# Kernel tuning notes

Measured on AMD Instinct MI355X. Metric: run time of the kernel, lower is better.

Reference implementation:

```python
import jax, jax.numpy as jnp
import numpy as np
import math

VOCAB, D, H, L = 32000, 1024, 16, 4
HD = D // H
DFF = 4 * D
EPS = 1e-5


def setup_inputs() -> dict:
    key = jax.random.key(0)
    ks = jax.random.split(key, 20)
    B, T = 4, 1024
    s = 0.02
    inp = {
        'inputs': jax.random.randint(ks[0], (B, T), 0, VOCAB),
        'emb_table': jax.random.normal(ks[1], (VOCAB, D), jnp.float32) * s,
        'Wq': jax.random.normal(ks[2], (L, D, D), jnp.float32) * s,
        'bq': jnp.zeros((L, D), jnp.float32),
        'Wk': jax.random.normal(ks[3], (L, D, D), jnp.float32) * s,
        'bk': jnp.zeros((L, D), jnp.float32),
        'Wv': jax.random.normal(ks[4], (L, D, D), jnp.float32) * s,
        'bv': jnp.zeros((L, D), jnp.float32),
        'Wo': jax.random.normal(ks[5], (L, D, D), jnp.float32) * s,
        'bo': jnp.zeros((L, D), jnp.float32),
        'ln1_g': jnp.ones((L, D), jnp.float32),
        'ln1_b': jnp.zeros((L, D), jnp.float32),
        'W1': jax.random.normal(ks[6], (L, D, DFF), jnp.float32) * s,
        'b1': jnp.zeros((L, DFF), jnp.float32),
        'W2': jax.random.normal(ks[7], (L, DFF, D), jnp.float32) * s,
        'b2': jnp.zeros((L, D), jnp.float32),
        'ln2_g': jnp.ones((L, D), jnp.float32),
        'ln2_b': jnp.zeros((L, D), jnp.float32),
    }
    return inp


def _layernorm(x, g, b):
    mu = jnp.mean(x, axis=-1, keepdims=True)
    var = jnp.mean(jnp.square(x - mu), axis=-1, keepdims=True)
    return (x - mu) * jax.lax.rsqrt(var + EPS) * g + b


def _pos_emb(T):
    pos = jnp.arange(T, dtype=jnp.float32)[:, None]          # [T,1]
    div = jnp.exp(jnp.arange(0, D, 2, dtype=jnp.float32) * (-math.log(10000.0) / D))
    pe = jnp.zeros((T, D), jnp.float32)
    pe = pe.at[:, 0::2].set(jnp.sin(pos * div))
    pe = pe.at[:, 1::2].set(jnp.cos(pos * div))
    return pe


def reference(inputs, emb_table, Wq, bq, Wk, bk, Wv, bv, Wo, bo,
              ln1_g, ln1_b, W1, b1, W2, b2, ln2_g, ln2_b):
    B, T = inputs.shape
    x = emb_table[inputs] + _pos_emb(T)[None, :, :]          # [B,T,D]
    causal = jnp.tril(jnp.ones((T, T), bool))                # [T,T]
    scale = 1.0 / math.sqrt(HD)
    for l in range(L):
        q = (x @ Wq[l] + bq[l]).reshape(B, T, H, HD)
        k = (x @ Wk[l] + bk[l]).reshape(B, T, H, HD)
        v = (x @ Wv[l] + bv[l]).reshape(B, T, H, HD)
        scores = jnp.einsum('bqhd,bkhd->bhqk', q, k) * scale
        scores = jnp.where(causal, scores, -jnp.inf)
        w = jax.nn.softmax(scores, axis=-1)
        attn = jnp.einsum('bhqk,bkhd->bqhd', w, v).reshape(B, T, D)
        attn = attn @ Wo[l] + bo[l]
        x = _layernorm(x + attn, ln1_g[l], ln1_b[l])
        ff = jax.nn.relu(x @ W1[l] + b1[l]) @ W2[l] + b2[l]
        x = _layernorm(x + ff, ln2_g[l], ln2_b[l])
    return x
```

## Files before the change

### kernel.cpp

```cpp
#include <hip/hip_runtime.h>

typedef __attribute__((ext_vector_type(8))) __bf16 bf16x8;
typedef __attribute__((ext_vector_type(4))) float f32x4;
typedef __attribute__((ext_vector_type(8))) unsigned short ushort8;

#define DMODEL 1024
#define SEQ 1024
#define NLAYER 4

__device__ __forceinline__ unsigned short f2bf(float f) {
  unsigned u = __float_as_uint(f);
  u += 0x7fffu + ((u >> 16) & 1u);
  return (unsigned short)(u >> 16);
}

__device__ __forceinline__ float bf2f(unsigned short u) {
  return __uint_as_float((unsigned)u << 16);
}

__device__ __forceinline__ void async_copy16(const void* gsrc, const void* lds_dst) {
  __builtin_amdgcn_global_load_lds(
      (__attribute__((address_space(1))) void*)(unsigned long long)(gsrc),
      (__attribute__((address_space(3))) void*)(unsigned int)(unsigned long long)(lds_dst),
      16, 0, 0);
}

__device__ __forceinline__ f32x4 mfma16(bf16x8 a, bf16x8 b, f32x4 c) {
  return __builtin_amdgcn_mfma_f32_16x16x32_bf16(a, b, c, 0, 0, 0);
}

__global__ __launch_bounds__(256) void preproc_kernel(
    const int* __restrict__ tok, const float* __restrict__ emb,
    const float* __restrict__ Wq, const float* __restrict__ Wk,
    const float* __restrict__ Wv, const float* __restrict__ Wo,
    const float* __restrict__ W1, const float* __restrict__ W2,
    const float* __restrict__ bq, const float* __restrict__ bk,
    const float* __restrict__ bv,
    unsigned short* __restrict__ wqkv_t, unsigned short* __restrict__ wo_t,
    unsigned short* __restrict__ w1_t, unsigned short* __restrict__ w2_t,
    float* __restrict__ qkvb, unsigned short* __restrict__ xb) {
  __shared__ unsigned short tileT[64 * 136];
  const int bid = blockIdx.x;
  const int tid = threadIdx.x;
  if (bid < 6144) {
    const float* src; unsigned short* dst; size_t R, C; int tx, ty;
    if (bid < 2048) {
      int w = bid >> 9, z = (bid >> 7) & 3, tl = bid & 127;
      tx = tl & 15; ty = tl >> 4; R = 1024; C = 1024;
      if (w == 0)      { src = Wq + (size_t)z * 1048576; dst = wqkv_t + (size_t)z * 3145728; }
      else if (w == 1) { src = Wk + (size_t)z * 1048576; dst = wqkv_t + (size_t)z * 3145728 + 1048576; }
      else if (w == 2) { src = Wv + (size_t)z * 1048576; dst = wqkv_t + (size_t)z * 3145728 + 2097152; }
      else             { src = Wo + (size_t)z * 1048576; dst = wo_t + (size_t)z * 1048576; }
    } else if (bid < 4096) {
      int t = bid - 2048, z = t >> 9, tl = t & 511;
      tx = tl & 63; ty = tl >> 6; R = 1024; C = 4096;
      src = W1 + (size_t)z * 4194304; dst = w1_t + (size_t)z * 4194304;
    } else {
      int t = bid - 4096, z = t >> 9, tl = t & 511;
      tx = tl & 15; ty = tl >> 4; R = 4096; C = 1024;
      src = W2 + (size_t)z * 4194304; dst = w2_t + (size_t)z * 4194304;
    }
    const int c0 = tx * 64, r0 = ty * 128;
    const int s16 = tid & 15, hi = tid >> 4;
#pragma unroll
    for (int it = 0; it < 8; ++it) {
      const int r = it * 16 + hi;
      f32x4 v = __builtin_nontemporal_load(
          (const f32x4*)(src + (size_t)(r0 + r) * C + c0 + s16 * 4));
#pragma unroll
      for (int j = 0; j < 4; ++j) {
        const int c = s16 * 4 + j;
        tileT[c * 136 + (r ^ ((c & 7) << 3))] = f2bf(v[j]);
      }
    }
    __syncthreads();
#pragma unroll
    for (int p = 0; p < 4; ++p) {
      const int c = p * 16 + hi;
      ushort8 o = *(const ushort8*)&tileT[c * 136 + 8 * (s16 ^ (c & 7))];
      *(ushort8*)(dst + (size_t)(c0 + c) * R + r0 + s16 * 8) = o;
    }
  } else if (bid < 10240) {
    const int row = bid - 6144;
    const int t = row & (SEQ - 1);
    const int tk = tok[row];
    const int col = tid * 4;
    float4 e = *(const float4*)(emb + (size_t)tk * DMODEL + col);
    const float c = -9.21034037197618f / (float)DMODEL;
    float d0 = __expf((float)(col)*c);
    float d1 = __expf((float)(col + 2) * c);
    float a0 = (float)t * d0, a1 = (float)t * d1;
    e.x += sinf(a0); e.y += cosf(a0); e.z += sinf(a1); e.w += cosf(a1);
    ushort4 ub;
    ub.x = f2bf(e.x); ub.y = f2bf(e.y); ub.z = f2bf(e.z); ub.w = f2bf(e.w);
    *(ushort4*)(xb + (size_t)row * DMODEL + col) = ub;
  } else {
    int i = (bid - 10240) * 256 + tid;
    if (i < NLAYER * 3072) {
      int l = i / 3072, j = i % 3072;
      float v = (j < 1024) ? bq[l * 1024 + j]
              : (j < 2048) ? bk[l * 1024 + j - 1024]
                           : bv[l * 1024 + j - 2048];
      qkvb[i] = v;
    }
  }
}

#define G256_PHASE(BUF, MH, NH, STAGE_STMT, VM)                                   \
  {                                                                               \
    if (NH == 0) {                                                                \
      _Pragma("unroll") for (int fm = 0; fm < 4; ++fm)                            \
      _Pragma("unroll") for (int kk = 0; kk < 2; ++kk) {                          \
        int row = wr * 64 + fm * 16 + lr;                                         \
        int cb = (kk * 64 + g * 16) ^ ((row & 4) ? 32 : 0) ^ ((row & 8) ? 64 : 0);\
        af[fm][kk] = *(const bf16x8*)((const char*)&As[BUF][MH][0] + row * 128 + cb); \
      }                                                                           \
    }                                                                             \
    _Pragma("unroll") for (int fn = 0; fn < 2; ++fn)                              \
    _Pragma("unroll") for (int kk = 0; kk < 2; ++kk) {                            \
      int row = wc * 32 + fn * 16 + lr;                                           \
      int cb = (kk * 64 + g * 16) ^ ((row & 4) ? 32 : 0) ^ ((row & 8) ? 64 : 0);  \
      bfr[fn][kk] = *(const bf16x8*)((const char*)&Bs[BUF][NH][0] + row * 128 + cb); \
    }                                                                             \
    STAGE_STMT;                                                                   \
    if (VM == 1) asm volatile("s_waitcnt vmcnt(4)" ::: "memory");                 \
    if (VM == 2) asm volatile("s_waitcnt vmcnt(0)" ::: "memory");                 \
    asm volatile("s_barrier" ::: "memory");                                       \
    asm volatile("s_waitcnt lgkmcnt(0)" ::: "memory");                            \
    __builtin_amdgcn_s_setprio(1);                                                \
    _Pragma("unroll") for (int fm = 0; fm < 4; ++fm)                              \
    _Pragma("unroll") for (int fn = 0; fn < 2; ++fn)                              \
    _Pragma("unroll") for (int kk = 0; kk < 2; ++kk)                              \
      acc[MH][fm][NH][fn] = mfma16(af[fm][kk], bfr[fn][kk], acc[MH][fm][NH][fn]); \
    __builtin_amdgcn_s_setprio(0);                                                \
    asm volatile("s_barrier" ::: "memory");                                       \
  }

template <int QKV>
__global__ __launch_bounds__(512, 1) void gemm256(
    const unsigned short* __restrict__ A, const unsigned short* __restrict__ Bt,
    const float* __restrict__ bias, unsigned short* __restrict__ Cb,
    unsigned short* __restrict__ Cb2, int N) {
  __shared__ __align__(16) unsigned short As[2][2][8192];
  __shared__ __align__(16) unsigned short Bs[2][2][8192];
  constexpr int NK = 16;
  constexpr int NI = 8;

  const int tid = threadIdx.x;
  const int wid = tid >> 6, l = tid & 63;
  const int lr = l & 15, g = l >> 4;
  const int wr = wid >> 2, wc = wid & 3;

  const int gx = gridDim.x, nwg = gx * gridDim.y;
  int bid = blockIdx.y * gx + blockIdx.x;
  const int cpx = nwg >> 3;
  bid = (bid & 7) * cpx + (bid >> 3);
  const int rm = (bid / gx) * 256, rn = (bid % gx) * 256;

  const int kOff = ((l & 7) * 8) ^ ((l & 32) ? 16 : 0) ^ ((wid & 1) ? 32 : 0);
  const int rOff = wid * 8 + (l >> 3);

  auto stA = [&](int buf, int half, int t) {
#pragma unroll
    for (int r2 = 0; r2 < 2; ++r2) {
      const unsigned short* gs =
          A + (size_t)(rm + half * 128 + r2 * 64 + rOff) * 1024 + t * 64 + kOff;
      async_copy16(gs, &As[buf][half][r2 * 4096 + wid * 512]);
    }
  };
  auto stB = [&](int buf, int half, int t) {
#pragma unroll
    for (int r2 = 0; r2 < 2; ++r2) {
      const unsigned short* gs =
          Bt + (size_t)(rn + half * 128 + r2 * 64 + rOff) * 1024 + t * 64 + kOff;
      async_copy16(gs, &Bs[buf][half][r2 * 4096 + wid * 512]);
    }
  };

  f32x4 acc[2][4][2][2] = {};
  bf16x8 af[4][2], bfr[2][2];

  stA(0, 0, 0); stA(0, 1, 0); stB(0, 0, 0); stB(0, 1, 0);
  stA(1, 0, 1); stB(1, 0, 1);
  asm volatile("s_waitcnt vmcnt(4)" ::: "memory");
  asm volatile("s_barrier" ::: "memory");

  for (int i = 0; i < NI - 1; ++i) {
    const int t1 = 2 * i + 1, t2 = 2 * i + 2, t3 = 2 * i + 3;
    G256_PHASE(0, 0, 0, { stA(1, 1, t1); }, 0)
    G256_PHASE(0, 0, 1, { stB(1, 1, t1); }, 0)
    G256_PHASE(0, 1, 0, { stA(0, 0, t2); }, 0)
    G256_PHASE(0, 1, 1, { stB(0, 0, t2); }, 1)
    G256_PHASE(1, 0, 0, { stA(0, 1, t2); }, 0)
    G256_PHASE(1, 0, 1, { stB(0, 1, t2); }, 0)
    G256_PHASE(1, 1, 0, { if (t3 < NK) stA(1, 0, t3); }, 0)
    G256_PHASE(1, 1, 1, { if (t3 < NK) stB(1, 0, t3); }, 1)
  }
  {
    const int t1 = NK - 1;
    G256_PHASE(0, 0, 0, { stA(1, 1, t1); }, 0)
    G256_PHASE(0, 0, 1, { stB(1, 1, t1); }, 0)
    G256_PHASE(0, 1, 0, {}, 0)
    G256_PHASE(0, 1, 1, {}, 2)
    G256_PHASE(1, 0, 0, {}, 0)
    G256_PHASE(1, 0, 1, {}, 0)
    G256_PHASE(1, 1, 0, {}, 0)
    G256_PHASE(1, 1, 1, {}, 0)
  }

#pragma unroll
  for (int mh = 0; mh < 2; ++mh)
#pragma unroll
    for (int nh = 0; nh < 2; ++nh)
#pragma unroll
      for (int fn = 0; fn < 2; ++fn) {
        const int col = rn + nh * 128 + wc * 32 + fn * 16 + lr;
        const float bv = bias[col];
        if (QKV && col >= 2048) {
#pragma unroll
          for (int fm = 0; fm < 4; ++fm) {
            const int row0 = rm + mh * 128 + wr * 64 + fm * 16 + g * 4;
            ushort4 vv;
            vv.x = f2bf(acc[mh][fm][nh][fn][0] + bv);
            vv.y = f2bf(acc[mh][fm][nh][fn][1] + bv);
            vv.z = f2bf(acc[mh][fm][nh][fn][2] + bv);
            vv.w = f2bf(acc[mh][fm][nh][fn][3] + bv);
            *(ushort4*)(Cb2 + (size_t)(col - 2048) * 4096 + row0) = vv;
          }
        } else {
          const float sc = (QKV && col < 1024) ? 0.18033688011112042f : 1.0f;
          const int ldc = QKV ? 2048 : N;
#pragma unroll
          for (int fm = 0; fm < 4; ++fm)
#pragma unroll
            for (int r = 0; r < 4; ++r) {
              const int row = rm + mh * 128 + wr * 64 + fm * 16 + g * 4 + r;
              float v = (acc[mh][fm][nh][fn][r] + bv) * sc;
              if (!QKV) v = fmaxf(v, 0.0f);
              Cb[(size_t)row * ldc + col] = f2bf(v);
            }
        }
      }
}

__global__ __launch_bounds__(512, 4) void gemm_bf16w(
    const unsigned short* __restrict__ A, const unsigned short* __restrict__ Bt,
    const float* __restrict__ bias, unsigned short* __restrict__ Cb,
    const unsigned short* __restrict__ Xres, int N, int K) {
  __shared__ __align__(16) unsigned short As[2][8192];
  __shared__ __align__(16) unsigned short Bs[2][8192];
  const int tid = threadIdx.x;
  const int wid = tid >> 6, l = tid & 63, lr = l & 15, g = l >> 4;
  const int wr = wid >> 2, wc = wid & 3;
  const int d = blockIdx.y * 8 + blockIdx.x;
  const int xcd = d & 7, slot = d >> 3;
  const int bandsPerXcd = gridDim.y >> 3;
  const int by = xcd * bandsPerXcd + (slot >> 3);
  const int bx = slot & 7;
  const int rm = by * 128, rn = bx * 128;
  const int nk = K >> 6;

  const int kOff = ((l & 7) * 8) ^ ((l & 32) ? 16 : 0) ^ ((wid & 1) ? 32 : 0);
  const int rOff = wid * 8 + (l >> 3);

  auto stage = [&](int buf, int t) {
#pragma unroll
    for (int r2 = 0; r2 < 2; ++r2) {
      const unsigned short* ga =
          A + (size_t)(rm + r2 * 64 + rOff) * K + t * 64 + kOff;
      async_copy16(ga, &As[buf][r2 * 4096 + wid * 512]);
      const unsigned short* gb =
          Bt + (size_t)(rn + r2 * 64 + rOff) * K + t * 64 + kOff;
      async_copy16(gb, &Bs[buf][r2 * 4096 + wid * 512]);
    }
  };

  f32x4 acc[4][2] = {};
  stage(0, 0);
  asm volatile("s_waitcnt vmcnt(0)" ::: "memory");
  asm volatile("s_barrier" ::: "memory");

  for (int t = 0; t < nk; ++t) {
    const int cur = t & 1;
    if (t + 1 < nk) stage(cur ^ 1, t + 1);
    bf16x8 af[4][2], bfr[2][2];
#pragma unroll
    for (int fm = 0; fm < 4; ++fm)
#pragma unroll
      for (int kk = 0; kk < 2; ++kk) {
        int row = wr * 64 + fm * 16 + lr;
        int cb = (kk * 64 + g * 16) ^ ((row & 4) ? 32 : 0) ^ ((row & 8) ? 64 : 0);
        af[fm][kk] = *(const bf16x8*)((const char*)&As[cur][0] + row * 128 + cb);
      }
#pragma unroll
    for (int fn = 0; fn < 2; ++fn)
#pragma unroll
      for (int kk = 0; kk < 2; ++kk) {
        int row = wc * 32 + fn * 16 + lr;
        int cb = (kk * 64 + g * 16) ^ ((row & 4) ? 32 : 0) ^ ((row & 8) ? 64 : 0);
        bfr[fn][kk] = *(const bf16x8*)((const char*)&Bs[cur][0] + row * 128 + cb);
      }
    asm volatile("s_waitcnt lgkmcnt(0)" ::: "memory");
    __builtin_amdgcn_sched_barrier(0);
    __builtin_amdgcn_s_setprio(1);
#pragma unroll
    for (int fm = 0; fm < 4; ++fm)
#pragma unroll
      for (int fn = 0; fn < 2; ++fn)
#pragma unroll
        for (int kk = 0; kk < 2; ++kk)
          acc[fm][fn] = mfma16(af[fm][kk], bfr[fn][kk], acc[fm][fn]);
    __builtin_amdgcn_s_setprio(0);
    asm volatile("s_waitcnt vmcnt(0)" ::: "memory");
    asm volatile("s_barrier" ::: "memory");
  }

  const int row0 = rm + wr * 64 + g * 4;
  const int col0 = rn + wc * 32 + lr;
#pragma unroll
  for (int fn = 0; fn < 2; ++fn) {
    const int col = col0 + fn * 16;
    const float bv = bias[col];
#pragma unroll
    for (int fm = 0; fm < 4; ++fm)
#pragma unroll
      for (int r = 0; r < 4; ++r) {
        const int row = row0 + fm * 16 + r;
        float v = acc[fm][fn][r] + bv + bf2f(Xres[(size_t)row * N + col]);
        Cb[(size_t)row * N + col] = f2bf(v);
      }
  }
}

__global__ __launch_bounds__(256) void attn_kernel(
    const unsigned short* __restrict__ qk, const unsigned short* __restrict__ Vt,
    unsigned short* __restrict__ out) {
  __shared__ unsigned short Pl[4][32 * 72];
  const int tid = threadIdx.x;
  const int w = tid >> 6, lr = tid & 15, g = (tid & 63) >> 4;
  const int bh = blockIdx.x;
  const int b = bh >> 4, h = bh & 15;
  const int byy = blockIdx.y;
  const int qblk = (byy < 4) ? (7 - byy) : (byy - 4);
  const int qb0 = qblk * 128 + w * 32;
  const size_t rowBase = (size_t)b * SEQ;
  const int cq = h * 64, ck = 1024 + h * 64;
  const unsigned short* Vb = Vt + (size_t)(h * 64) * 4096 + b * 1024;

  bf16x8 aq[2][2];
#pragma unroll
  for (int qf = 0; qf < 2; ++qf)
#pragma unroll
    for (int ks = 0; ks < 2; ++ks)
      aq[qf][ks] = *(const bf16x8*)(qk + (rowBase + qb0 + qf * 16 + lr) * 2048 +
                                    cq + ks * 32 + g * 8);

  f32x4 o[2][4] = {};
  float l_[2][4] = {};

  const int NT = (qb0 + 32 + 63) >> 6;

  bf16x8 kf[4][2];
#pragma unroll
  for (int kg = 0; kg < 4; ++kg) {
    const unsigned short* kp = qk + (rowBase + kg * 16 + lr) * 2048 + ck + g * 8;
    kf[kg][0] = *(const bf16x8*)(kp);
    kf[kg][1] = *(const bf16x8*)(kp + 32);
  }

  for (int kt = 0; kt < NT; ++kt) {
    const int k0 = kt * 64;
    bf16x8 vf[4][2];
#pragma unroll
    for (int nbv = 0; nbv < 4; ++nbv) {
      const unsigned short* vp = Vb + (size_t)(nbv * 16 + lr) * 4096 + k0 + g * 8;
      vf[nbv][0] = *(const bf16x8*)(vp);
      vf[nbv][1] = *(const bf16x8*)(vp + 32);
    }
    f32x4 s[2][4] = {};
#pragma unroll
    for (int kg = 0; kg < 4; ++kg)
#pragma unroll
      for (int qf = 0; qf < 2; ++qf) {
        s[qf][kg] = mfma16(aq[qf][0], kf[kg][0], s[qf][kg]);
        s[qf][kg] = mfma16(aq[qf][1], kf[kg][1], s[qf][kg]);
      }
    if (kt + 1 < NT) {
#pragma unroll
      for (int kg = 0; kg < 4; ++kg) {
        const unsigned short* kp =
            qk + (rowBase + k0 + 64 + kg * 16 + lr) * 2048 + ck + g * 8;
        kf[kg][0] = *(const bf16x8*)(kp);
        kf[kg][1] = *(const bf16x8*)(kp + 32);
      }
    }
    if (k0 + 63 <= qb0) {
#pragma unroll
      for (int qf = 0; qf < 2; ++qf)
#pragma unroll
        for (int r = 0; r < 4; ++r) {
          float e0 = exp2f(s[qf][0][r]);
          float e1 = exp2f(s[qf][1][r]);
          float e2 = exp2f(s[qf][2][r]);
          float e3 = exp2f(s[qf][3][r]);
          l_[qf][r] += (e0 + e1) + (e2 + e3);
          unsigned short* pr = &Pl[w][(qf * 16 + g * 4 + r) * 72];
          pr[lr] = f2bf(e0);
          pr[16 + lr] = f2bf(e1);
          pr[32 + lr] = f2bf(e2);
          pr[48 + lr] = f2bf(e3);
        }
    } else {
#pragma unroll
      for (int qf = 0; qf < 2; ++qf)
#pragma unroll
        for (int r = 0; r < 4; ++r) {
          const int q = qb0 + qf * 16 + g * 4 + r;
          float e0 = (k0 + lr <= q) ? exp2f(s[qf][0][r]) : 0.0f;
          float e1 = (k0 + 16 + lr <= q) ? exp2f(s[qf][1][r]) : 0.0f;
          float e2 = (k0 + 32 + lr <= q) ? exp2f(s[qf][2][r]) : 0.0f;
          float e3 = (k0 + 48 + lr <= q) ? exp2f(s[qf][3][r]) : 0.0f;
          l_[qf][r] += (e0 + e1) + (e2 + e3);
          unsigned short* pr = &Pl[w][(qf * 16 + g * 4 + r) * 72];
          pr[lr] = f2bf(e0);
          pr[16 + lr] = f2bf(e1);
          pr[32 + lr] = f2bf(e2);
          pr[48 + lr] = f2bf(e3);
        }
    }
    asm volatile("s_waitcnt lgkmcnt(0)" ::: "memory");
    __builtin_amdgcn_sched_barrier(0);
    bf16x8 pa[2][2];
#pragma unroll
    for (int qf = 0; qf < 2; ++qf)
#pragma unroll
      for (int kc = 0; kc < 2; ++kc)
        pa[qf][kc] = *(const bf16x8*)&Pl[w][(qf * 16 + lr) * 72 + kc * 32 + g * 8];
#pragma unroll
    for (int nbv = 0; nbv < 4; ++nbv)
#pragma unroll
      for (int qf = 0; qf < 2; ++qf) {
        o[qf][nbv] = mfma16(pa[qf][0], vf[nbv][0], o[qf][nbv]);
        o[qf][nbv] = mfma16(pa[qf][1], vf[nbv][1], o[qf][nbv]);
      }
  }
  float rinv[2][4];
#pragma unroll
  for (int qf = 0; qf < 2; ++qf)
#pragma unroll
    for (int r = 0; r < 4; ++r) {
      float t = l_[qf][r];
      t += __shfl_xor(t, 1, 64);
      t += __shfl_xor(t, 2, 64);
      t += __shfl_xor(t, 4, 64);
      t += __shfl_xor(t, 8, 64);
      rinv[qf][r] = __builtin_amdgcn_rcpf(t);
    }
#pragma unroll
  for (int qf = 0; qf < 2; ++qf)
#pragma unroll
    for (int nbv = 0; nbv < 4; ++nbv)
#pragma unroll
      for (int r = 0; r < 4; ++r) {
        float val = o[qf][nbv][r] * rinv[qf][r];
        out[(rowBase + qb0 + qf * 16 + g * 4 + r) * 1024 + h * 64 + nbv * 16 + lr] =
            f2bf(val);
      }
}

__global__ __launch_bounds__(256) void ln_kernel(
    const unsigned short* __restrict__ tin,
    const float* __restrict__ gam, const float* __restrict__ bet,
    unsigned short* __restrict__ xbf, float* __restrict__ out2) {
  const int w = threadIdx.x >> 6, lane = threadIdx.x & 63;
  const int row = blockIdx.x * 4 + w;
  const size_t base = (size_t)row * DMODEL;
  const int c0 = lane * 8;
  const int c1 = 512 + lane * 8;
  ushort8 u0 = *(const ushort8*)(tin + base + c0);
  ushort8 u1 = *(const ushort8*)(tin + base + c1);
  float v[16];
#pragma unroll
  for (int i = 0; i < 8; ++i) { v[i] = bf2f(u0[i]); v[8 + i] = bf2f(u1[i]); }
  float s = 0.0f, ss = 0.0f;
#pragma unroll
  for (int i = 0; i < 16; ++i) { s += v[i]; ss += v[i] * v[i]; }
#pragma unroll
  for (int msk = 32; msk; msk >>= 1) {
    s += __shfl_xor(s, msk, 64);
    ss += __shfl_xor(ss, msk, 64);
  }
  const float mean = s * (1.0f / DMODEL);
  const float var = ss * (1.0f / DMODEL) - mean * mean;
  const float inv = rsqrtf(var + 1e-5f);
  float gv[16], bv[16];
  *(float4*)(gv + 0) = *(const float4*)(gam + c0);
  *(float4*)(gv + 4) = *(const float4*)(gam + c0 + 4);
  *(float4*)(gv + 8) = *(const float4*)(gam + c1);
  *(float4*)(gv + 12) = *(const float4*)(gam + c1 + 4);
  *(float4*)(bv + 0) = *(const float4*)(bet + c0);
  *(float4*)(bv + 4) = *(const float4*)(bet + c0 + 4);
  *(float4*)(bv + 8) = *(const float4*)(bet + c1);
  *(float4*)(bv + 12) = *(const float4*)(bet + c1 + 4);
  float ov[16];
#pragma unroll
  for (int i = 0; i < 16; ++i) ov[i] = (v[i] - mean) * inv * gv[i] + bv[i];
  ushort8 o0, o1;
#pragma unroll
  for (int i = 0; i < 8; ++i) { o0[i] = f2bf(ov[i]); o1[i] = f2bf(ov[8 + i]); }
  *(ushort8*)(xbf + base + c0) = o0;
  *(ushort8*)(xbf + base + c1) = o1;
  if (out2) {
    *(float4*)(out2 + base + c0) = *(float4*)(ov + 0);
    *(float4*)(out2 + base + c0 + 4) = *(float4*)(ov + 4);
    *(float4*)(out2 + base + c1) = *(float4*)(ov + 8);
    *(float4*)(out2 + base + c1 + 4) = *(float4*)(ov + 12);
  }
}

extern "C" void kernel_launch(void* const* d_in, const int* in_sizes, int n_in,
                              void* d_out, int out_size, void* d_ws, size_t ws_size,
                              hipStream_t stream) {
  (void)in_sizes; (void)n_in; (void)out_size; (void)ws_size;
  const int* tok = (const int*)d_in[0];
  const float* emb = (const float*)d_in[1];
  const float* Wq = (const float*)d_in[2];
  const float* bq = (const float*)d_in[3];
  const float* Wk = (const float*)d_in[4];
  const float* bk = (const float*)d_in[5];
  const float* Wv = (const float*)d_in[6];
  const float* bv = (const float*)d_in[7];
  const float* Wo = (const float*)d_in[8];
  const float* bo = (const float*)d_in[9];
  const float* ln1g = (const float*)d_in[10];
  const float* ln1b = (const float*)d_in[11];
  const float* W1 = (const float*)d_in[12];
  const float* b1 = (const float*)d_in[13];
  const float* W2 = (const float*)d_in[14];
  const float* b2 = (const float*)d_in[15];
  const float* ln2g = (const float*)d_in[16];
  const float* ln2b = (const float*)d_in[17];

  char* ws = (char*)d_ws;
  size_t off = 0;
  auto alloc = [&](size_t bytes) {
    char* p = ws + off;
    off += (bytes + 255) & ~(size_t)255;
    return p;
  };
  unsigned short* wqkv_t = (unsigned short*)alloc((size_t)NLAYER * 3072 * 1024 * 2);
  unsigned short* wo_t = (unsigned short*)alloc((size_t)NLAYER * 1024 * 1024 * 2);
  unsigned short* w1_t = (unsigned short*)alloc((size_t)NLAYER * 4096 * 1024 * 2);
  unsigned short* w2_t = (unsigned short*)alloc((size_t)NLAYER * 1024 * 4096 * 2);
  float* qkvb = (float*)alloc((size_t)NLAYER * 3072 * 4);
  unsigned short* yb = (unsigned short*)alloc((size_t)4096 * 1024 * 2);
  unsigned short* xb = (unsigned short*)alloc((size_t)4096 * 1024 * 2);
  unsigned short* qkbuf = (unsigned short*)alloc((size_t)4096 * 2048 * 2);
  unsigned short* vt = (unsigned short*)alloc((size_t)1024 * 4096 * 2);
  unsigned short* attn = (unsigned short*)alloc((size_t)4096 * 1024 * 2);
  unsigned short* hb = (unsigned short*)alloc((size_t)4096 * 4096 * 2);

  preproc_kernel<<<dim3(10288), dim3(256), 0, stream>>>(
      tok, emb, Wq, Wk, Wv, Wo, W1, W2, bq, bk, bv,
      wqkv_t, wo_t, w1_t, w2_t, qkvb, xb);

  for (int l = 0; l < NLAYER; ++l) {
    gemm256<1><<<dim3(12, 16), dim3(512), 0, stream>>>(
        xb, wqkv_t + (size_t)l * 3145728, qkvb + l * 3072, qkbuf, vt, 3072);
    attn_kernel<<<dim3(64, 8), dim3(256), 0, stream>>>(qkbuf, vt, attn);
    gemm_bf16w<<<dim3(8, 32), dim3(512), 0, stream>>>(
        attn, wo_t + (size_t)l * 1048576, bo + l * 1024, yb, xb, 1024, 1024);
    ln_kernel<<<dim3(1024), dim3(256), 0, stream>>>(
        yb, ln1g + l * 1024, ln1b + l * 1024, xb, nullptr);
    gemm256<0><<<dim3(16, 16), dim3(512), 0, stream>>>(
        xb, w1_t + (size_t)l * 4194304, b1 + l * 4096, hb, nullptr, 4096);
    gemm_bf16w<<<dim3(8, 32), dim3(512), 0, stream>>>(
        hb, w2_t + (size_t)l * 4194304, b2 + l * 1024, yb, xb, 1024, 4096);
    ln_kernel<<<dim3(1024), dim3(256), 0, stream>>>(
        yb, ln2g + l * 1024, ln2b + l * 1024, xb,
        (l == NLAYER - 1) ? (float*)d_out : nullptr);
  }
}
```

Baseline: 827.4 us.

## Stage attention K/V tiles in double-buffered swizzled LDS shared by all waves

Previously each of the four waves in an attention block loaded the same K and V tiles from global memory straight into registers. Now the block loads each 64x64 K and V tile once into LDS with async global-to-LDS copies, using an XOR swizzle and double buffering so the next tile is fetched while the current one is computed. Each wave then reads its fragments from LDS. This cuts redundant global/L2 traffic for K/V. In exchange it adds a block-wide barrier per tile and makes every wave run the block's full tile count, so waves with earlier query rows compute extra fully masked tiles.

```diff
diff --git a/kernel.cpp b/kernel.cpp
--- a/kernel.cpp
+++ b/kernel.cpp
@@ -335,9 +335,11 @@
 __global__ __launch_bounds__(256) void attn_kernel(
     const unsigned short* __restrict__ qk, const unsigned short* __restrict__ Vt,
     unsigned short* __restrict__ out) {
+  __shared__ __align__(16) unsigned short Ks[2][64 * 64];
+  __shared__ __align__(16) unsigned short Vs[2][64 * 64];
   __shared__ unsigned short Pl[4][32 * 72];
   const int tid = threadIdx.x;
-  const int w = tid >> 6, lr = tid & 15, g = (tid & 63) >> 4;
+  const int w = tid >> 6, l = tid & 63, lr = l & 15, g = l >> 4;
   const int bh = blockIdx.x;
   const int b = bh >> 4, h = bh & 15;
   const int byy = blockIdx.y;
@@ -345,7 +347,24 @@
   const int qb0 = qblk * 128 + w * 32;
   const size_t rowBase = (size_t)b * SEQ;
   const int cq = h * 64, ck = 1024 + h * 64;
-  const unsigned short* Vb = Vt + (size_t)(h * 64) * 4096 + b * 1024;
+  const int NTb = 2 * qblk + 2;
+
+  const int sOff = ((l & 7) * 8) ^ ((l & 32) ? 16 : 0);
+  const int sRow = l >> 3;
+
+  auto stageKV = [&](int buf, int t) {
+#pragma unroll
+    for (int j = 0; j < 2; ++j) {
+      const int row = w * 16 + j * 8 + sRow;
+      const int off = sOff ^ (j ? 32 : 0);
+      const unsigned short* gk =
+          qk + (rowBase + t * 64 + row) * 2048 + ck + off;
+      async_copy16(gk, &Ks[buf][(w * 16 + j * 8) * 64]);
+      const unsigned short* gv =
+          Vt + (size_t)(h * 64 + row) * 4096 + b * 1024 + t * 64 + off;
+      async_copy16(gv, &Vs[buf][(w * 16 + j * 8) * 64]);
+    }
+  };
 
   bf16x8 aq[2][2];
 #pragma unroll
@@ -358,25 +377,23 @@
   f32x4 o[2][4] = {};
   float l_[2][4] = {};
 
-  const int NT = (qb0 + 32 + 63) >> 6;
-
-  bf16x8 kf[4][2];
-#pragma unroll
-  for (int kg = 0; kg < 4; ++kg) {
-    const unsigned short* kp = qk + (rowBase + kg * 16 + lr) * 2048 + ck + g * 8;
-    kf[kg][0] = *(const bf16x8*)(kp);
-    kf[kg][1] = *(const bf16x8*)(kp + 32);
-  }
-
-  for (int kt = 0; kt < NT; ++kt) {
+  const int rdswz = ((lr & 4) ? 16 : 0) ^ ((lr & 8) ? 32 : 0);
+
+  stageKV(0, 0);
+  asm volatile("s_waitcnt vmcnt(0)" ::: "memory");
+  asm volatile("s_barrier" ::: "memory");
+
+  for (int kt = 0; kt < NTb; ++kt) {
     const int k0 = kt * 64;
-    bf16x8 vf[4][2];
-#pragma unroll
-    for (int nbv = 0; nbv < 4; ++nbv) {
-      const unsigned short* vp = Vb + (size_t)(nbv * 16 + lr) * 4096 + k0 + g * 8;
-      vf[nbv][0] = *(const bf16x8*)(vp);
-      vf[nbv][1] = *(const bf16x8*)(vp + 32);
-    }
+    const int cur = kt & 1;
+    if (kt + 1 < NTb) stageKV(cur ^ 1, kt + 1);
+    bf16x8 kf[4][2];
+#pragma unroll
+    for (int kg = 0; kg < 4; ++kg)
+#pragma unroll
+      for (int ks = 0; ks < 2; ++ks)
+        kf[kg][ks] = *(const bf16x8*)&Ks[cur][(kg * 16 + lr) * 64 +
+                                             ((ks * 32 + g * 8) ^ rdswz)];
     f32x4 s[2][4] = {};
 #pragma unroll
     for (int kg = 0; kg < 4; ++kg)
@@ -385,15 +402,6 @@
         s[qf][kg] = mfma16(aq[qf][0], kf[kg][0], s[qf][kg]);
         s[qf][kg] = mfma16(aq[qf][1], kf[kg][1], s[qf][kg]);
       }
-    if (kt + 1 < NT) {
-#pragma unroll
-      for (int kg = 0; kg < 4; ++kg) {
-        const unsigned short* kp =
-            qk + (rowBase + k0 + 64 + kg * 16 + lr) * 2048 + ck + g * 8;
-        kf[kg][0] = *(const bf16x8*)(kp);
-        kf[kg][1] = *(const bf16x8*)(kp + 32);
-      }
-    }
     if (k0 + 63 <= qb0) {
 #pragma unroll
       for (int qf = 0; qf < 2; ++qf)
@@ -436,6 +444,13 @@
 #pragma unroll
       for (int kc = 0; kc < 2; ++kc)
         pa[qf][kc] = *(const bf16x8*)&Pl[w][(qf * 16 + lr) * 72 + kc * 32 + g * 8];
+    bf16x8 vf[4][2];
+#pragma unroll
+    for (int nbv = 0; nbv < 4; ++nbv)
+#pragma unroll
+      for (int ks = 0; ks < 2; ++ks)
+        vf[nbv][ks] = *(const bf16x8*)&Vs[cur][(nbv * 16 + lr) * 64 +
+                                               ((ks * 32 + g * 8) ^ rdswz)];
 #pragma unroll
     for (int nbv = 0; nbv < 4; ++nbv)
 #pragma unroll
@@ -443,6 +458,8 @@
         o[qf][nbv] = mfma16(pa[qf][0], vf[nbv][0], o[qf][nbv]);
         o[qf][nbv] = mfma16(pa[qf][1], vf[nbv][1], o[qf][nbv]);
       }
+    asm volatile("s_waitcnt vmcnt(0)" ::: "memory");
+    asm volatile("s_barrier" ::: "memory");
   }
   float rinv[2][4];
 #pragma unroll
```

Result: faster. 798.4 us (-3.5%).
